# Kernel tuning notes

Hardware: AMD Instinct MI355X
Metric: run time of the kernel (lower is better)

## Reference

```python
import jax, jax.numpy as jnp
import numpy as np

GROUP_SIZE = 16
E2M1_MAX = 6.0
# Positive E2M1 grid and midpoints for round-to-nearest
E2M1_POS = jnp.array([0.0, 0.5, 1.0, 1.5, 2.0, 3.0, 4.0, 6.0], jnp.float32)
E2M1_MID = jnp.array([0.25, 0.75, 1.25, 1.75, 2.5, 3.5, 5.0], jnp.float32)
# Full 16-entry signed LUT (bit3 = sign, sign-magnitude)
E2M1_LUT = jnp.array([0.0, 0.5, 1.0, 1.5, 2.0, 3.0, 4.0, 6.0,
                      -0.0, -0.5, -1.0, -1.5, -2.0, -3.0, -4.0, -6.0], jnp.float32)

def _round_e2m1(x):
    # nearest value on the E2M1 grid (clamped to +-6)
    idx = jnp.searchsorted(E2M1_MID, jnp.abs(x))
    return jnp.sign(x) * E2M1_POS[idx]

def nvfp4_act_qdq(x, input_scale):
    # per-group dynamic quantize to NVFP4 with fp8-e4m3 group scale, then dequantize
    orig_shape = x.shape
    xg = x.astype(jnp.float32).reshape(*orig_shape[:-1], -1, GROUP_SIZE)
    amax = jnp.max(jnp.abs(xg), axis=-1, keepdims=True)
    s = (amax / (E2M1_MAX * input_scale)).astype(jnp.float8_e4m3fn).astype(jnp.float32)
    s = jnp.where(s > 0, s, 1.0)
    total = s * input_scale  # effective per-group scale
    dq = _round_e2m1(xg / total) * total
    return dq.reshape(orig_shape).astype(jnp.float16)

def nvfp4_dequantize(weight, weight_scale, weight_scale_2):
    # weight: [O, I//2] packed bytes (values 0..255); low nibble = even index
    O = weight.shape[0]
    low = weight & 0xF
    high = (weight >> 4) & 0xF
    codes = jnp.stack([low, high], axis=-1).reshape(O, -1)  # [O, I]
    vals = E2M1_LUT[codes].reshape(O, -1, GROUP_SIZE)       # [O, G, 16]
    w = vals * weight_scale[:, :, None] * weight_scale_2
    return w.reshape(O, -1).astype(jnp.float16)

def setup_inputs() -> dict:
    key = jax.random.key(0)
    k1, k2, k3 = jax.random.split(key, 3)
    B, S, I, O = 8, 16, 8192, 8192
    hidden_states = jax.random.normal(k1, (B, S, I), dtype=jnp.float16)
    weight = jax.random.randint(k2, (O, I // 2), 0, 256, dtype=jnp.int32)
    weight_scale = jax.random.uniform(k3, (O, I // GROUP_SIZE), dtype=jnp.float32) * 0.05 + 0.001
    weight_scale_2 = jnp.ones((1,), jnp.float32)
    input_scale = jnp.ones((1,), jnp.float32)
    return {"hidden_states": hidden_states, "weight": weight,
            "weight_scale": weight_scale, "weight_scale_2": weight_scale_2,
            "input_scale": input_scale}

def reference(hidden_states, weight, weight_scale, weight_scale_2, input_scale):
    hs_dq = nvfp4_act_qdq(hidden_states, input_scale)
    w_dq = nvfp4_dequantize(weight, weight_scale, weight_scale_2)
    return jnp.matmul(hs_dq, w_dq.T)  # [B, S, O], fp16
```

## Files before the change

### kernel.cpp

```cpp
#include <hip/hip_runtime.h>
#include <stdint.h>


typedef _Float16 half8 __attribute__((ext_vector_type(8)));
typedef float float4v __attribute__((ext_vector_type(4)));

__device__ __forceinline__ uint32_t perm_b32(uint32_t hi, uint32_t lo, uint32_t sel) {
  return __builtin_amdgcn_perm(hi, lo, sel);
}

__device__ __forceinline__ float e4m3_roundtrip(float x) {
  if (x < 0.015625f) {
    return __builtin_rintf(x * 512.0f) * 0.001953125f;
  }
  uint32_t u = __float_as_uint(x);
  u += 0x7FFFFu + ((u >> 20) & 1u);
  u &= 0xFFF00000u;
  float y = __uint_as_float(u);
  return fminf(y, 448.0f);
}

__global__ __launch_bounds__(256)
void aqdq_kernel(const float* __restrict__ hs,
                 const float* __restrict__ isc,
                 uint2* __restrict__ asw) {
  const int t = blockIdx.x * 256 + threadIdx.x;
  const int m = t >> 11;
  const int u = t & 2047;
  const int g = u >> 2;
  const int hq = u & 3;

  const float* p = hs + m * 8192 + g * 16 + hq * 4;
  float4 x = *(const float4*)p;

  float amax = fmaxf(fmaxf(fabsf(x.x), fabsf(x.y)), fmaxf(fabsf(x.z), fabsf(x.w)));
  amax = fmaxf(amax, __shfl_xor(amax, 1));
  amax = fmaxf(amax, __shfl_xor(amax, 2));

  float is = isc[0];
  float s = e4m3_roundtrip(amax / (6.0f * is));
  if (!(s > 0.0f)) s = 1.0f;
  float total = s * is;

  float xv[4] = {x.x, x.y, x.z, x.w};
  union { _Float16 h[4]; uint2 v; } qq;
#pragma unroll
  for (int i = 0; i < 4; ++i) {
    float r = xv[i] / total;
    float a = fabsf(r);
    float v = (a <= 0.25f) ? 0.0f
            : (a <= 0.75f) ? 0.5f
            : (a <= 1.25f) ? 1.0f
            : (a <= 1.75f) ? 1.5f
            : (a <= 2.5f)  ? 2.0f
            : (a <= 3.5f)  ? 3.0f
            : (a <= 5.0f)  ? 4.0f : 6.0f;
    qq.h[i] = (_Float16)(copysignf(v, r) * total);
  }

  const int k = g * 16 + hq * 4;
  const int kb = k >> 5;
  const int quad = (k >> 3) & 3;
  const int lane16 = (m & 15) | (quad << 4);
  const int mb = m >> 4;
  asw[((kb * 8 + mb) * 64 + lane16) * 2 + (hq & 1)] = qq.v;
}

__device__ __forceinline__ half8 decode_scale(int4 w, float sf) {
  uint32_t t0 = perm_b32((uint32_t)w.y, (uint32_t)w.x, 0x00000400u);
  uint32_t t1 = perm_b32((uint32_t)w.w, (uint32_t)w.z, 0x04000000u);
  uint32_t b  = perm_b32(t1, t0, 0x07060100u);
  uint32_t ev = b & 0x0F0F0F0Fu;
  uint32_t od = (b >> 4) & 0x0F0F0F0Fu;
  uint32_t evm = ev & 0x07070707u;
  uint32_t odm = od & 0x07070707u;
  uint32_t evs = (ev & 0x08080808u) << 4;
  uint32_t ods = (od & 0x08080808u) << 4;
  uint32_t evh = perm_b32(0x46444240u, 0x3E3C3800u, evm) | evs;
  uint32_t odh = perm_b32(0x46444240u, 0x3E3C3800u, odm) | ods;
  union { uint32_t u[4]; half8 h; } r;
  r.u[0] = perm_b32(odh, evh, 0x04000000u) & 0xFF00FF00u;
  r.u[1] = perm_b32(odh, evh, 0x05000100u) & 0xFF00FF00u;
  r.u[2] = perm_b32(odh, evh, 0x06000200u) & 0xFF00FF00u;
  r.u[3] = perm_b32(odh, evh, 0x07000300u) & 0xFF00FF00u;
  _Float16 hsf = (_Float16)sf;
  half8 sv = {hsf, hsf, hsf, hsf, hsf, hsf, hsf, hsf};
  return r.h * sv;
}

__global__ __launch_bounds__(512, 4)
void gemm_kernel(const uint4* __restrict__ asw,
                 const int* __restrict__ wq,
                 const float* __restrict__ wsc,
                 const float* __restrict__ ws2p,
                 float* __restrict__ out) {
  __shared__ float red[8][16][132];
  const int lane = threadIdx.x & 63;
  const int wv = threadIdx.x >> 6;
  const int quad = lane >> 4;
  const int n0 = blockIdx.x * 16;
  const int rA = n0 + (lane & 15);
  const float ws2 = ws2p[0];
  const int4* wpA = (const int4*)(wq + rA * 4096);
  const float* wsA = wsc + rA * 512;
  const int kbase = wv * 1024;

  float4v acc[8];
#pragma unroll
  for (int mb = 0; mb < 8; ++mb) acc[mb] = (float4v){0.f, 0.f, 0.f, 0.f};

  const uint4* ap = asw + (kbase >> 5) * 512 + lane;

#pragma unroll 2
  for (int ks = 0; ks < 32; ++ks) {
    const int k0 = kbase + ks * 32;
    int4 wA = wpA[(k0 >> 3) + quad];
    float2 sv = *(const float2*)(wsA + (k0 >> 4));
    float sA = ((quad & 2) ? sv.y : sv.x) * ws2;
    uint4 af[8];
#pragma unroll
    for (int mb = 0; mb < 8; ++mb) af[mb] = ap[ks * 512 + mb * 64];
    half8 bA = decode_scale(wA, sA);
#pragma unroll
    for (int mb = 0; mb < 8; ++mb) {
      union { uint4 u; half8 h; } a;
      a.u = af[mb];
      acc[mb] = __builtin_amdgcn_mfma_f32_16x16x32_f16(a.h, bA, acc[mb], 0, 0, 0);
    }
  }

#pragma unroll
  for (int mb = 0; mb < 8; ++mb) {
    *(float4v*)&red[wv][lane & 15][mb * 16 + quad * 4] = acc[mb];
  }
  __syncthreads();

  const int t = threadIdx.x;
  const int m = t >> 2;
  const int j0 = (t & 3) * 4;
  float o[4];
#pragma unroll
  for (int j = 0; j < 4; ++j) {
    float s = 0.f;
#pragma unroll
    for (int p = 0; p < 8; ++p) s += red[p][j0 + j][m];
    o[j] = s;
  }
  *(float4*)&out[m * 8192 + n0 + j0] = *(float4*)&o[0];
}

extern "C" void kernel_launch(void* const* d_in, const int* in_sizes, int n_in,
                              void* d_out, int out_size, void* d_ws, size_t ws_size,
                              hipStream_t stream) {
  (void)in_sizes; (void)n_in; (void)out_size; (void)ws_size;
  const float* hs  = (const float*)d_in[0];
  const int* wq    = (const int*)d_in[1];
  const float* wsc = (const float*)d_in[2];
  const float* ws2 = (const float*)d_in[3];
  const float* isc = (const float*)d_in[4];
  float* out       = (float*)d_out;
  uint2* asw2      = (uint2*)d_ws;
  const uint4* asw4 = (const uint4*)d_ws;

  aqdq_kernel<<<1024, 256, 0, stream>>>(hs, isc, asw2);
  gemm_kernel<<<512, 512, 0, stream>>>(asw4, wq, wsc, ws2, out);
}
```

Baseline: 265.4 us.

## Share activation tiles via LDS double buffer and split K across blocks

Each block now covers 128 output columns (8 waves × 16) over one eighth of K, instead of 16 columns over all of K. Activation fragments are loaded once per block into a double-buffered LDS tile and shared by all waves, with weights and scales for the next step prefetched while the current step computes. Partial sums go to a workspace followed by a separate reduce kernel, or to atomic adds if the workspace is too small. This cuts redundant activation reads but adds per-step barriers, 32 MB of partial-sum traffic and an extra kernel launch.

```diff
diff --git a/kernel.cpp b/kernel.cpp
--- a/kernel.cpp
+++ b/kernel.cpp
@@ -88,71 +88,98 @@
   return r.h * sv;
 }
 
+template<int MODE>
 __global__ __launch_bounds__(512, 4)
 void gemm_kernel(const uint4* __restrict__ asw,
                  const int* __restrict__ wq,
                  const float* __restrict__ wsc,
                  const float* __restrict__ ws2p,
-                 float* __restrict__ out) {
-  __shared__ float red[8][16][132];
+                 float* __restrict__ dst) {
+  __shared__ uint4 abuf[2][8][64];
   const int lane = threadIdx.x & 63;
   const int wv = threadIdx.x >> 6;
   const int quad = lane >> 4;
-  const int n0 = blockIdx.x * 16;
-  const int rA = n0 + (lane & 15);
+  const int kp = blockIdx.x & 7;
+  const int nb = blockIdx.x >> 3;
+  const int col = nb * 128 + wv * 16 + (lane & 15);
   const float ws2 = ws2p[0];
-  const int4* wpA = (const int4*)(wq + rA * 4096);
-  const float* wsA = wsc + rA * 512;
-  const int kbase = wv * 1024;
+  const int4* wp = (const int4*)(wq + (size_t)col * 4096) + kp * 128 + quad;
+  const float2* sp = (const float2*)(wsc + (size_t)col * 512 + kp * 64);
+  const uint4* ap = asw + kp * 16384 + wv * 64 + lane;
 
   float4v acc[8];
 #pragma unroll
   for (int mb = 0; mb < 8; ++mb) acc[mb] = (float4v){0.f, 0.f, 0.f, 0.f};
 
-  const uint4* ap = asw + (kbase >> 5) * 512 + lane;
-
-#pragma unroll 2
-  for (int ks = 0; ks < 32; ++ks) {
-    const int k0 = kbase + ks * 32;
-    int4 wA = wpA[(k0 >> 3) + quad];
-    float2 sv = *(const float2*)(wsA + (k0 >> 4));
-    float sA = ((quad & 2) ? sv.y : sv.x) * ws2;
-    uint4 af[8];
-#pragma unroll
-    for (int mb = 0; mb < 8; ++mb) af[mb] = ap[ks * 512 + mb * 64];
-    half8 bA = decode_scale(wA, sA);
+  {
+    uint4 a0 = ap[0];
+    int4 w0 = wp[0];
+    float2 s0 = sp[0];
+    abuf[0][wv][lane] = a0;
+    __syncthreads();
+    int4 wC = w0; float2 sC = s0;
+    for (int t = 0; t < 32; ++t) {
+      uint4 aN; int4 wN; float2 sN;
+      const bool more = (t < 31);
+      if (more) {
+        aN = ap[(t + 1) * 512];
+        wN = wp[(t + 1) * 4];
+        sN = sp[t + 1];
+      }
+      uint4 af[8];
+#pragma unroll
+      for (int mb = 0; mb < 8; ++mb) af[mb] = abuf[t & 1][mb][lane];
+      float sA = ((quad & 2) ? sC.y : sC.x) * ws2;
+      half8 bA = decode_scale(wC, sA);
+#pragma unroll
+      for (int mb = 0; mb < 8; ++mb) {
+        union { uint4 u; half8 h; } a;
+        a.u = af[mb];
+        acc[mb] = __builtin_amdgcn_mfma_f32_16x16x32_f16(a.h, bA, acc[mb], 0, 0, 0);
+      }
+      if (more) {
+        abuf[(t + 1) & 1][wv][lane] = aN;
+        __syncthreads();
+        wC = wN; sC = sN;
+      }
+    }
+  }
+
+  if (MODE == 0) {
+    float* pp = dst + ((size_t)kp << 20) + col;
 #pragma unroll
     for (int mb = 0; mb < 8; ++mb) {
-      union { uint4 u; half8 h; } a;
-      a.u = af[mb];
-      acc[mb] = __builtin_amdgcn_mfma_f32_16x16x32_f16(a.h, bA, acc[mb], 0, 0, 0);
+      const int mrow = mb * 16 + quad * 4;
+#pragma unroll
+      for (int r = 0; r < 4; ++r) pp[(size_t)(mrow + r) * 8192] = acc[mb][r];
     }
-  }
-
-#pragma unroll
-  for (int mb = 0; mb < 8; ++mb) {
-    *(float4v*)&red[wv][lane & 15][mb * 16 + quad * 4] = acc[mb];
-  }
-  __syncthreads();
-
-  const int t = threadIdx.x;
-  const int m = t >> 2;
-  const int j0 = (t & 3) * 4;
-  float o[4];
-#pragma unroll
-  for (int j = 0; j < 4; ++j) {
-    float s = 0.f;
-#pragma unroll
-    for (int p = 0; p < 8; ++p) s += red[p][j0 + j][m];
-    o[j] = s;
-  }
-  *(float4*)&out[m * 8192 + n0 + j0] = *(float4*)&o[0];
+  } else {
+#pragma unroll
+    for (int mb = 0; mb < 8; ++mb) {
+      const int mrow = mb * 16 + quad * 4;
+#pragma unroll
+      for (int r = 0; r < 4; ++r)
+        unsafeAtomicAdd(&dst[(size_t)(mrow + r) * 8192 + col], acc[mb][r]);
+    }
+  }
+}
+
+__global__ __launch_bounds__(256)
+void reduce_kernel(const float4* __restrict__ part, float4* __restrict__ out) {
+  const int i = blockIdx.x * 256 + threadIdx.x;
+  float4 s = part[i];
+#pragma unroll
+  for (int p = 1; p < 8; ++p) {
+    float4 b = part[(size_t)p * 262144 + i];
+    s.x += b.x; s.y += b.y; s.z += b.z; s.w += b.w;
+  }
+  out[i] = s;
 }
 
 extern "C" void kernel_launch(void* const* d_in, const int* in_sizes, int n_in,
                               void* d_out, int out_size, void* d_ws, size_t ws_size,
                               hipStream_t stream) {
-  (void)in_sizes; (void)n_in; (void)out_size; (void)ws_size;
+  (void)in_sizes; (void)n_in; (void)out_size;
   const float* hs  = (const float*)d_in[0];
   const int* wq    = (const int*)d_in[1];
   const float* wsc = (const float*)d_in[2];
@@ -163,5 +190,14 @@
   const uint4* asw4 = (const uint4*)d_ws;
 
   aqdq_kernel<<<1024, 256, 0, stream>>>(hs, isc, asw2);
-  gemm_kernel<<<512, 512, 0, stream>>>(asw4, wq, wsc, ws2, out);
-}
+
+  const size_t need = ((size_t)2 << 20) + ((size_t)32 << 20);
+  if (ws_size >= need) {
+    float* part = (float*)((char*)d_ws + ((size_t)2 << 20));
+    gemm_kernel<0><<<512, 512, 0, stream>>>(asw4, wq, wsc, ws2, part);
+    reduce_kernel<<<1024, 256, 0, stream>>>((const float4*)part, (float4*)out);
+  } else {
+    hipMemsetAsync(out, 0, (size_t)128 * 8192 * 4, stream);
+    gemm_kernel<1><<<512, 512, 0, stream>>>(asw4, wq, wsc, ws2, out);
+  }
+}
```

Result: faster. 241.9 us (-8.9%).
